# Kernel optimization log

Measured on AMD Instinct MI355X. Metric: run time of the kernel, lower is better.

The kernel has to match this reference:

```python
import jax, jax.numpy as jnp
import numpy as np

W_DIM = 72  # positional_encoding(3 coords, 12 freqs) -> 3*12*2
_F1 = np.array([1.0, 3.0, 3.0, 1.0], dtype=np.float32)
_F2 = np.outer(_F1, _F1); _F2 = _F2 / _F2.sum()  # normalized StyleGAN resample filter


def upsample2x(x):
    """Antialiased 2x upsample: zero-insertion + 4-tap [1,3,3,1] FIR, gain=4 (upfirdn2d)."""
    C = x.shape[1]
    k = jnp.tile(jnp.asarray(_F2 * 4.0, x.dtype)[None, None], (C, 1, 1, 1))  # [C,1,4,4]
    return jax.lax.conv_general_dilated(
        x, k, (1, 1), ((2, 2), (2, 2)), lhs_dilation=(2, 2),
        feature_group_count=C, dimension_numbers=('NCHW', 'OIHW', 'NCHW'))


def affine(w_vec, aw, ab):
    # FullyConnectedLayer: runtime weight gain 1/sqrt(w_dim), bias init 1
    return (w_vec @ aw.T) / np.sqrt(W_DIM) + ab


def mod_conv(x, weight, styles, demodulate=True, padding=1):
    """StyleGAN2 modulated conv2d (batch=1). weight [Co,Ci,k,k], styles [Ci]."""
    w = weight * styles[None, :, None, None]
    if demodulate:
        d = jax.lax.rsqrt(jnp.sum(w * w, axis=(1, 2, 3)) + 1e-8)
        w = w * d[:, None, None, None]
    return jax.lax.conv_general_dilated(
        x, w, (1, 1), ((padding, padding), (padding, padding)),
        dimension_numbers=('NCHW', 'OIHW', 'NCHW'))


def syn_layer(x, w_vec, aw, ab, cw, cb, up):
    s = affine(w_vec, aw, ab)
    if up:
        x = upsample2x(x)
    x = mod_conv(x, cw, s, True, 1)
    # bias_act: lrelu, gain sqrt(2), conv_clamp 256 (noise_strength init 0 -> no noise)
    x = jax.nn.leaky_relu(x + cb[None, :, None, None], 0.2) * np.sqrt(2.0)
    return jnp.clip(x, -256.0, 256.0)


def to_rgb(x, w_vec, aw, ab, cw, cb):
    s = affine(w_vec, aw, ab) / np.sqrt(cw.shape[1])  # ToRGB weight_gain 1/sqrt(Cin)
    y = mod_conv(x, cw, s, False, 0)
    return jnp.clip(y + cb[None, :, None, None], -256.0, 256.0)


def reference(rays, rgbs, conv_w, conv_b, bn_gamma, bn_beta, bn_mean, bn_var,
              a0_w, a0_b, w0, b0, a1_w, a1_b, w1, b1, t0_aw, t0_ab, t0_w, t0_b,
              a2_w, a2_b, w2, b2, a3_w, a3_b, w3, b3, t1_aw, t1_ab, t1_w, t1_b):
    # style vector from positional encoding of ray origin
    p = rays[0, :3, 0, 0]
    fb = 2.0 ** jnp.arange(12, dtype=rays.dtype)
    pts = (p[:, None] * fb[None, :]).reshape(-1)  # (36,)
    w_vec = jnp.concatenate([jnp.sin(pts), jnp.cos(pts)])  # (72,)
    # mapping: 1x1 conv + relu + BatchNorm2d (eval-mode)
    feat = jnp.einsum('oi,bihw->bohw', conv_w[:, :, 0, 0], rgbs) + conv_b[None, :, None, None]
    feat = jax.nn.relu(feat)
    inv = jax.lax.rsqrt(bn_var + 1e-5)
    feat = (feat - bn_mean[None, :, None, None]) * (inv * bn_gamma)[None, :, None, None] + bn_beta[None, :, None, None]
    rgb = feat[:, :3]
    # block0: 32ch@128 -> 256ch@256, skip-architecture ToRGB
    x = syn_layer(feat, w_vec, a0_w, a0_b, w0, b0, True)
    x = syn_layer(x, w_vec, a1_w, a1_b, w1, b1, False)
    img = upsample2x(rgb) + to_rgb(x, w_vec, t0_aw, t0_ab, t0_w, t0_b)
    # block1: 256ch@256 -> 128ch@512
    x = syn_layer(x, w_vec, a2_w, a2_b, w2, b2, True)
    x = syn_layer(x, w_vec, a3_w, a3_b, w3, b3, False)
    img = upsample2x(img) + to_rgb(x, w_vec, t1_aw, t1_ab, t1_w, t1_b)
    return img  # [1,3,512,512]


def setup_inputs() -> dict:
    key = jax.random.key(0)
    ks = jax.random.split(key, 16)
    rn = lambda k, s: jax.random.normal(k, s, dtype=jnp.float32)
    z = lambda s: jnp.zeros(s, jnp.float32)
    o = lambda s: jnp.ones(s, jnp.float32)
    inp = {}
    inp['rays'] = rn(ks[0], (1, 6, 128, 128))
    inp['rgbs'] = jax.random.uniform(ks[1], (1, 3, 128, 128), dtype=jnp.float32)
    inp['conv_w'] = rn(ks[2], (32, 3, 1, 1)); inp['conv_b'] = z((32,))
    inp['bn_gamma'] = o((32,)); inp['bn_beta'] = z((32,))
    inp['bn_mean'] = z((32,)); inp['bn_var'] = o((32,))
    inp['a0_w'] = rn(ks[3], (32, 72)); inp['a0_b'] = o((32,))
    inp['w0'] = rn(ks[4], (256, 32, 3, 3)); inp['b0'] = z((256,))
    inp['a1_w'] = rn(ks[5], (256, 72)); inp['a1_b'] = o((256,))
    inp['w1'] = rn(ks[6], (256, 256, 3, 3)); inp['b1'] = z((256,))
    inp['t0_aw'] = rn(ks[7], (256, 72)); inp['t0_ab'] = o((256,))
    inp['t0_w'] = rn(ks[8], (3, 256, 1, 1)); inp['t0_b'] = z((3,))
    inp['a2_w'] = rn(ks[9], (256, 72)); inp['a2_b'] = o((256,))
    inp['w2'] = rn(ks[10], (128, 256, 3, 3)); inp['b2'] = z((128,))
    inp['a3_w'] = rn(ks[11], (128, 72)); inp['a3_b'] = o((128,))
    inp['w3'] = rn(ks[12], (128, 128, 3, 3)); inp['b3'] = z((128,))
    inp['t1_aw'] = rn(ks[13], (128, 72)); inp['t1_ab'] = o((128,))
    inp['t1_w'] = rn(ks[14], (3, 128, 1, 1)); inp['t1_b'] = z((3,))
    return inp
```

## Files before the change

### kernel.cpp

```cpp
#include <hip/hip_runtime.h>
#include <cstddef>

typedef __attribute__((ext_vector_type(8))) short short8;
typedef __attribute__((ext_vector_type(4))) float f32x4;
typedef __attribute__((address_space(3))) void lds_void;
typedef const __attribute__((address_space(1))) void glob_void;

static const size_t OFF_S0    = 0;
static const size_t OFF_S1    = 64;
static const size_t OFF_S2    = 320;
static const size_t OFF_S3    = 576;
static const size_t OFF_MT0   = 704;
static const size_t OFF_MT1   = 1472;
static const size_t OFF_ZERO  = 1856;
static const size_t OFF_RGBF  = 2048;
static const size_t OFF_IMG0  = 51200;
static const size_t OFF_RGBP  = 247808;
static const size_t OFF_WQ0   = 1900544;
static const size_t OFF_WQ1   = 1937408;
static const size_t OFF_WQ2   = 2232320;
static const size_t OFF_WQ3   = 2379776;
static const size_t OFF_FEAT  = 2453504;
static const size_t OFF_UFEAT = 2715648;
static const size_t OFF_X1    = 4194304;
static const size_t OFF_X2    = 4194304;
static const size_t OFF_U     = 20971520;
static const size_t OFF_X0    = 20971520;

__device__ __forceinline__ unsigned short f2bf(float f) {
  unsigned int u = __float_as_uint(f);
  return (unsigned short)((u + 0x7FFFu + ((u >> 16) & 1u)) >> 16);
}
__device__ __forceinline__ float b2f(short h) {
  return __uint_as_float(((unsigned int)(unsigned short)h) << 16);
}

__global__ void __launch_bounds__(256) prep_kernel(
    const float* __restrict__ rays,
    const float* __restrict__ a0w, const float* __restrict__ a0b,
    const float* __restrict__ a1w, const float* __restrict__ a1b,
    const float* __restrict__ t0aw, const float* __restrict__ t0ab,
    const float* __restrict__ a2w, const float* __restrict__ a2b,
    const float* __restrict__ a3w, const float* __restrict__ a3b,
    const float* __restrict__ t1aw, const float* __restrict__ t1ab,
    const float* __restrict__ t0w, const float* __restrict__ t1w,
    float* __restrict__ ws)
{
  __shared__ float wv[72];
  __shared__ float st0l[256];
  __shared__ float st1l[128];
  const int tid = threadIdx.x;
  if (tid < 128) ws[OFF_ZERO + tid] = 0.f;
  if (tid < 36) {
    int i = tid / 12, j = tid % 12;
    float v = rays[i * 16384] * (float)(1 << j);
    wv[tid]      = sinf(v);
    wv[36 + tid] = cosf(v);
  }
  __syncthreads();
  const float inv72 = 0.11785113019775793f;

  if (tid < 32) {
    float d = 0.f;
    for (int k = 0; k < 72; ++k) d += wv[k] * a0w[tid * 72 + k];
    ws[OFF_S0 + tid] = fmaf(d, inv72, a0b[tid]);
  }
  {
    float d = 0.f;
    for (int k = 0; k < 72; ++k) d += wv[k] * a1w[tid * 72 + k];
    ws[OFF_S1 + tid] = fmaf(d, inv72, a1b[tid]);
  }
  {
    float d = 0.f;
    for (int k = 0; k < 72; ++k) d += wv[k] * t0aw[tid * 72 + k];
    st0l[tid] = fmaf(d, inv72, t0ab[tid]) * 0.0625f;
  }
  {
    float d = 0.f;
    for (int k = 0; k < 72; ++k) d += wv[k] * a2w[tid * 72 + k];
    ws[OFF_S2 + tid] = fmaf(d, inv72, a2b[tid]);
  }
  if (tid < 128) {
    float d = 0.f;
    for (int k = 0; k < 72; ++k) d += wv[k] * a3w[tid * 72 + k];
    ws[OFF_S3 + tid] = fmaf(d, inv72, a3b[tid]);
  }
  if (tid < 128) {
    float d = 0.f;
    for (int k = 0; k < 72; ++k) d += wv[k] * t1aw[tid * 72 + k];
    st1l[tid] = fmaf(d, inv72, t1ab[tid]) * 0.08838834764831845f;
  }
  __syncthreads();
  for (int i = tid; i < 768; i += 256) ws[OFF_MT0 + i] = t0w[i] * st0l[i & 255];
  for (int i = tid; i < 384; i += 256) ws[OFF_MT1 + i] = t1w[i] * st1l[i & 127];
}

__global__ void __launch_bounds__(256) modw_kernel(
    const float* __restrict__ w, const float* __restrict__ s,
    unsigned short* __restrict__ wq, int Ci, int Co)
{
  const int co = blockIdx.x;
  const int n = Ci * 9;
  float local = 0.f;
  for (int i = threadIdx.x; i < n; i += 256) {
    float v = w[co * n + i] * s[i / 9];
    local += v * v;
  }
#pragma unroll
  for (int off = 32; off >= 1; off >>= 1) local += __shfl_xor(local, off);
  __shared__ float red[4];
  if ((threadIdx.x & 63) == 0) red[threadIdx.x >> 6] = local;
  __syncthreads();
  const float d = rsqrtf(red[0] + red[1] + red[2] + red[3] + 1e-8f);
  const int sxor = (co & 3) ^ ((co >> 2) & 3);
  for (int i = threadIdx.x; i < n; i += 256) {
    int ci = i / 9, t = i - ci * 9;
    int kk = ci & 31;
    int sl = (kk >> 3) ^ sxor;
    wq[(((size_t)(ci >> 5) * 9 + t) * Co + co) * 32 + (sl << 3) + (kk & 7)] =
        f2bf(w[co * n + i] * s[ci] * d);
  }
}

__global__ void __launch_bounds__(256) feat_kernel(
    const float* __restrict__ rgbs, const float* __restrict__ cw, const float* __restrict__ cb,
    const float* __restrict__ gam, const float* __restrict__ bet,
    const float* __restrict__ mean, const float* __restrict__ var,
    unsigned short* __restrict__ feat, float* __restrict__ rgbf)
{
  const int p = blockIdx.x * 256 + threadIdx.x;
  const float r = rgbs[p], g = rgbs[16384 + p], b = rgbs[32768 + p];
  unsigned int pk[16];
#pragma unroll
  for (int co = 0; co < 32; ++co) {
    float v = cw[co * 3] * r + cw[co * 3 + 1] * g + cw[co * 3 + 2] * b + cb[co];
    v = fmaxf(v, 0.f);
    float inv = rsqrtf(var[co] + 1e-5f);
    v = (v - mean[co]) * (inv * gam[co]) + bet[co];
    if (co < 3) rgbf[co * 16384 + p] = v;
    unsigned int h = f2bf(v);
    if ((co & 1) == 0) pk[co >> 1] = h;
    else               pk[co >> 1] |= h << 16;
  }
  uint4* dst = reinterpret_cast<uint4*>(feat + (size_t)p * 32);
#pragma unroll
  for (int q = 0; q < 4; ++q)
    dst[q] = make_uint4(pk[q * 4], pk[q * 4 + 1], pk[q * 4 + 2], pk[q * 4 + 3]);
}

__global__ void __launch_bounds__(256) up2x_nhwc_kernel(
    const unsigned short* __restrict__ in, unsigned short* __restrict__ out,
    int H, int W, int c8s , int w2s )
{
  const int cid = blockIdx.x * 256 + threadIdx.x;
  const int k = cid & ((1 << c8s) - 1);
  const int pix = cid >> c8s;
  const int ey = pix >> w2s;
  const int ex = pix & ((1 << w2s) - 1);
  const int C = 8 << c8s;
  int ry0; float ay0, ay1;
  if (ey & 1) { ry0 = ey >> 1;       ay0 = 0.75f; ay1 = 0.25f; }
  else        { ry0 = (ey >> 1) - 1; ay0 = 0.25f; ay1 = 0.75f; }
  int cx0; float bx0, bx1;
  if (ex & 1) { cx0 = ex >> 1;       bx0 = 0.75f; bx1 = 0.25f; }
  else        { cx0 = (ex >> 1) - 1; bx0 = 0.25f; bx1 = 0.75f; }
  const short8 z = {0, 0, 0, 0, 0, 0, 0, 0};
  short8 v00 = z, v01 = z, v10 = z, v11 = z;
  const bool yo0 = (ry0 >= 0), yo1 = (ry0 + 1 < H);
  const bool xo0 = (cx0 >= 0), xo1 = (cx0 + 1 < W);
  if (yo0 && xo0) v00 = *reinterpret_cast<const short8*>(in + ((size_t)(ry0 * W + cx0) * C + k * 8));
  if (yo0 && xo1) v01 = *reinterpret_cast<const short8*>(in + ((size_t)(ry0 * W + cx0 + 1) * C + k * 8));
  if (yo1 && xo0) v10 = *reinterpret_cast<const short8*>(in + ((size_t)((ry0 + 1) * W + cx0) * C + k * 8));
  if (yo1 && xo1) v11 = *reinterpret_cast<const short8*>(in + ((size_t)((ry0 + 1) * W + cx0 + 1) * C + k * 8));
  unsigned int o[4];
#pragma unroll
  for (int j = 0; j < 8; ++j) {
    float f = ay0 * (bx0 * b2f(v00[j]) + bx1 * b2f(v01[j]))
            + ay1 * (bx0 * b2f(v10[j]) + bx1 * b2f(v11[j]));
    unsigned int h = f2bf(f);
    if ((j & 1) == 0) o[j >> 1] = h;
    else              o[j >> 1] |= h << 16;
  }
  *reinterpret_cast<uint4*>(out + (size_t)pix * C + k * 8) = make_uint4(o[0], o[1], o[2], o[3]);
}

template <bool FUSE_RGB>
__global__ void __launch_bounds__(512) conv3x3_mfma(
    const unsigned short* __restrict__ in,
    const unsigned short* __restrict__ wq,
    const float* __restrict__ bias,
    unsigned short* __restrict__ out,
    const float* __restrict__ rgbw,
    float* __restrict__ rgbp,
    const unsigned short* __restrict__ zpage,
    int H, int W, int Ci, int Co)
{
  const int tid  = threadIdx.x;
  const int lane = tid & 63;
  const int wv   = tid >> 6;
  const int wr   = wv & 3;
  const int wg   = wv >> 2;
  const int lo   = lane & 15, hi = lane >> 4;
  const int tpr  = W >> 4;
  const int T_y  = (blockIdx.x / tpr) << 5;
  const int T_x  = (blockIdx.x % tpr) << 4;
  const int cogB = blockIdx.y << 7;
  const int cog  = cogB + (wg << 6);

  __shared__ short8 xs[2][2448];
  __shared__ short8 wlds[2][1536];
  __shared__ float  rw[FUSE_RGB ? 384 : 4];

  if (FUSE_RGB) {
    for (int i = tid; i < 3 * Co; i += 512) rw[i] = rgbw[i];
  }

  f32x4 acc[4][8];
#pragma unroll
  for (int a = 0; a < 4; ++a)
#pragma unroll
    for (int b = 0; b < 8; ++b) acc[a][b] = (f32x4){0.f, 0.f, 0.f, 0.f};

  const unsigned short* gsrc[5];
#pragma unroll
  for (int j = 0; j < 5; ++j) {
    const int s = j * 512 + tid;
    const int pix = s >> 2, kslot = s & 3;
    const int rr = pix / 18, cc = pix - rr * 18;
    const int gy = T_y - 1 + rr, gx = T_x - 1 + cc;
    const int k = kslot ^ ((cc >> 1) & 3);
    const bool inb = (s < 2448) && gy >= 0 && gy < H && gx >= 0 && gx < W;
    gsrc[j] = inb ? (in + ((size_t)(gy * W + gx) * Ci + (k << 3))) : zpage;
  }

#define STAGE(c, buf)                                                              \
  {                                                                                \
    const int cb_ = (c) << 5;                                                      \
    _Pragma("unroll")                                                              \
    for (int j = 0; j < 4; ++j)                                                    \
      __builtin_amdgcn_global_load_lds((glob_void*)(gsrc[j] + cb_),                \
                                       (lds_void*)&xs[buf][j * 512 + tid], 16, 0, 0); \
    if (tid < 400)                                                                 \
      __builtin_amdgcn_global_load_lds((glob_void*)(gsrc[4] + cb_),                \
                                       (lds_void*)&xs[buf][2048 + tid], 16, 0, 0); \
  }

#define STAGE_W(C, KX, BUF)                                                        \
  {                                                                                \
    _Pragma("unroll")                                                              \
    for (int j = 0; j < 3; ++j) {                                                  \
      const unsigned short* src_ =                                                 \
          wq + ((size_t)((C) * 9 + j * 3 + (KX)) * Co + cogB) * 32 + tid * 8;      \
      __builtin_amdgcn_global_load_lds((glob_void*)src_,                           \
                                       (lds_void*)&wlds[BUF][(j << 9) + tid], 16, 0, 0); \
    }                                                                              \
  }

  const int sxa   = (lo & 3) ^ ((lo >> 2) & 3);
  const int wbase = (((wg << 6) + lo) << 2) + (hi ^ sxa);
#define ALOADW(SLOT, KY, BUF)                                                      \
  {                                                                                \
    _Pragma("unroll")                                                              \
    for (int cf = 0; cf < 4; ++cf)                                                 \
      apf[SLOT][cf] = wlds[BUF][((KY) << 9) + wbase + (cf << 6)];                  \
  }

#define MF(A, B, C) __builtin_amdgcn_mfma_f32_16x16x32_bf16(A, B, C, 0, 0, 0)

  STAGE(0, 0);
  STAGE_W(0, 0, 0);
  __syncthreads();

  const int nch = Ci >> 5;
  const int rstride = 72;
  int wb = 0;
  for (int c = 0; c < nch; ++c) {
    const int cur = c & 1;
#pragma unroll
    for (int g = 0; g < 3; ++g) {
      if (g < 2)             { STAGE_W(c, g + 1, wb ^ 1); }
      else if (c + 1 < nch)  { STAGE_W(c + 1, 0, wb ^ 1); }
      if (g == 0 && c + 1 < nch) STAGE(c + 1, cur ^ 1);

      const int tx2  = lo + g;
      const int xv_  = hi ^ ((tx2 >> 1) & 3);
      const int rowb = (((wr << 3) * 18 + tx2) << 2) + xv_;

      short8 q0 = xs[cur][rowb];
      short8 q1 = xs[cur][rowb + rstride];
      short8 q2 = xs[cur][rowb + 2 * rstride];
      short8 q3 = xs[cur][rowb + 3 * rstride];
      short8 q4 = xs[cur][rowb + 4 * rstride];
      short8 q5 = xs[cur][rowb + 5 * rstride];
      short8 q6 = xs[cur][rowb + 6 * rstride];
      short8 q7 = xs[cur][rowb + 7 * rstride];

      short8 apf[2][4];
      ALOADW(0, 0, wb);
      ALOADW(1, 1, wb);
#pragma unroll
      for (int cf = 0; cf < 4; ++cf) {
        acc[cf][0] = MF(apf[0][cf], q0, acc[cf][0]);
        acc[cf][1] = MF(apf[0][cf], q1, acc[cf][1]);
        acc[cf][2] = MF(apf[0][cf], q2, acc[cf][2]);
        acc[cf][3] = MF(apf[0][cf], q3, acc[cf][3]);
        acc[cf][4] = MF(apf[0][cf], q4, acc[cf][4]);
        acc[cf][5] = MF(apf[0][cf], q5, acc[cf][5]);
        acc[cf][6] = MF(apf[0][cf], q6, acc[cf][6]);
        acc[cf][7] = MF(apf[0][cf], q7, acc[cf][7]);
      }
      short8 q8 = xs[cur][rowb + 8 * rstride];
      ALOADW(0, 2, wb);
#pragma unroll
      for (int cf = 0; cf < 4; ++cf) {
        acc[cf][0] = MF(apf[1][cf], q1, acc[cf][0]);
        acc[cf][1] = MF(apf[1][cf], q2, acc[cf][1]);
        acc[cf][2] = MF(apf[1][cf], q3, acc[cf][2]);
        acc[cf][3] = MF(apf[1][cf], q4, acc[cf][3]);
        acc[cf][4] = MF(apf[1][cf], q5, acc[cf][4]);
        acc[cf][5] = MF(apf[1][cf], q6, acc[cf][5]);
        acc[cf][6] = MF(apf[1][cf], q7, acc[cf][6]);
        acc[cf][7] = MF(apf[1][cf], q8, acc[cf][7]);
      }
      short8 q9 = xs[cur][rowb + 9 * rstride];
#pragma unroll
      for (int cf = 0; cf < 4; ++cf) {
        acc[cf][0] = MF(apf[0][cf], q2, acc[cf][0]);
        acc[cf][1] = MF(apf[0][cf], q3, acc[cf][1]);
        acc[cf][2] = MF(apf[0][cf], q4, acc[cf][2]);
        acc[cf][3] = MF(apf[0][cf], q5, acc[cf][3]);
        acc[cf][4] = MF(apf[0][cf], q6, acc[cf][4]);
        acc[cf][5] = MF(apf[0][cf], q7, acc[cf][5]);
        acc[cf][6] = MF(apf[0][cf], q8, acc[cf][6]);
        acc[cf][7] = MF(apf[0][cf], q9, acc[cf][7]);
      }
      __syncthreads();
      wb ^= 1;
    }
  }
#undef STAGE
#undef STAGE_W
#undef ALOADW
#undef MF

  const float rt2 = 1.41421356237309515f;
#pragma unroll
  for (int r = 0; r < 8; ++r) {
    const int gy = T_y + (wr << 3) + r;
    const int gx = T_x + lo;
    if (!FUSE_RGB) {
#pragma unroll
      for (int cf = 0; cf < 4; ++cf) {
        const int cb = cog + (cf << 4) + (hi << 2);
        const f32x4 bi = *reinterpret_cast<const f32x4*>(bias + cb);
        unsigned short h[4];
#pragma unroll
        for (int reg = 0; reg < 4; ++reg) {
          float vv = acc[cf][r][reg] + bi[reg];
          vv = (vv >= 0.f) ? vv : 0.2f * vv;
          vv *= rt2;
          vv = fminf(fmaxf(vv, -256.f), 256.f);
          h[reg] = f2bf(vv);
        }
        uint2 pk;
        pk.x = (unsigned int)h[0] | ((unsigned int)h[1] << 16);
        pk.y = (unsigned int)h[2] | ((unsigned int)h[3] << 16);
        *reinterpret_cast<uint2*>(out + (size_t)(gy * W + gx) * Co + cb) = pk;
      }
    } else {
      float p0 = 0.f, p1 = 0.f, p2 = 0.f;
#pragma unroll
      for (int cf = 0; cf < 4; ++cf) {
        const int cb = cog + (cf << 4) + (hi << 2);
        const f32x4 bi = *reinterpret_cast<const f32x4*>(bias + cb);
#pragma unroll
        for (int reg = 0; reg < 4; ++reg) {
          float vv = acc[cf][r][reg] + bi[reg];
          vv = (vv >= 0.f) ? vv : 0.2f * vv;
          vv *= rt2;
          vv = fminf(fmaxf(vv, -256.f), 256.f);
          p0 = fmaf(rw[cb + reg], vv, p0);
          p1 = fmaf(rw[Co + cb + reg], vv, p1);
          p2 = fmaf(rw[2 * Co + cb + reg], vv, p2);
        }
      }
      p0 += __shfl_xor(p0, 16); p0 += __shfl_xor(p0, 32);
      p1 += __shfl_xor(p1, 16); p1 += __shfl_xor(p1, 32);
      p2 += __shfl_xor(p2, 16); p2 += __shfl_xor(p2, 32);
      if (hi == 0) {
        const size_t HWs = (size_t)H * W;
        const size_t px  = (size_t)gy * W + gx;
        rgbp[((size_t)wg * 3 + 0) * HWs + px] = p0;
        rgbp[((size_t)wg * 3 + 1) * HWs + px] = p1;
        rgbp[((size_t)wg * 3 + 2) * HWs + px] = p2;
      }
    }
  }
}

__device__ __forceinline__ float up2x_sample(const float* __restrict__ im, int H, int W,
                                             int oy, int ox)
{
  int my = oy >> 1, mx = ox >> 1;
  int ry0; float ay0, ay1;
  if (oy & 1) { ry0 = my;     ay0 = 0.75f; ay1 = 0.25f; }
  else        { ry0 = my - 1; ay0 = 0.25f; ay1 = 0.75f; }
  int cx0; float bx0, bx1;
  if (ox & 1) { cx0 = mx;     bx0 = 0.75f; bx1 = 0.25f; }
  else        { cx0 = mx - 1; bx0 = 0.25f; bx1 = 0.75f; }
  float v00 = (ry0 >= 0    && cx0 >= 0   ) ? im[ry0 * W + cx0]           : 0.f;
  float v01 = (ry0 >= 0    && cx0 + 1 < W) ? im[ry0 * W + cx0 + 1]       : 0.f;
  float v10 = (ry0 + 1 < H && cx0 >= 0   ) ? im[(ry0 + 1) * W + cx0]     : 0.f;
  float v11 = (ry0 + 1 < H && cx0 + 1 < W) ? im[(ry0 + 1) * W + cx0 + 1] : 0.f;
  return ay0 * (bx0 * v00 + bx1 * v01) + ay1 * (bx0 * v10 + bx1 * v11);
}

__global__ void __launch_bounds__(256) img0_kernel(
    const float* __restrict__ rgbf, const unsigned short* __restrict__ x1,
    const float* __restrict__ mt0g, const float* __restrict__ tb,
    float* __restrict__ img0)
{
  __shared__ float mt[768];
  const int tid = threadIdx.x;
  for (int i = tid; i < 768; i += 256) mt[i] = mt0g[i];
  __syncthreads();
  const int p = blockIdx.x * 256 + tid;
  const unsigned short* xp = x1 + (size_t)p * 256;
  float a0 = 0.f, a1 = 0.f, a2 = 0.f;
  for (int i8 = 0; i8 < 32; ++i8) {
    const short8 v = *reinterpret_cast<const short8*>(xp + i8 * 8);
#pragma unroll
    for (int j = 0; j < 8; ++j) {
      const float xv = b2f(v[j]);
      const int ci = i8 * 8 + j;
      a0 = fmaf(mt[ci],       xv, a0);
      a1 = fmaf(mt[256 + ci], xv, a1);
      a2 = fmaf(mt[512 + ci], xv, a2);
    }
  }
  const int oy = p >> 8, ox = p & 255;
  float av[3] = {a0, a1, a2};
#pragma unroll
  for (int o = 0; o < 3; ++o) {
    float y = fminf(fmaxf(av[o] + tb[o], -256.f), 256.f);
    img0[o * 65536 + p] = up2x_sample(rgbf + o * 16384, 128, 128, oy, ox) + y;
  }
}

__global__ void __launch_bounds__(256) final_kernel(
    const float* __restrict__ img0, const float* __restrict__ rgbp,
    const float* __restrict__ tb, float* __restrict__ out)
{
  const int p = blockIdx.x * 256 + threadIdx.x;
  const int oy = p >> 9, ox = p & 511;
#pragma unroll
  for (int o = 0; o < 3; ++o) {
    float a = rgbp[(0 * 3 + o) * 262144 + p] + rgbp[(1 * 3 + o) * 262144 + p];
    float y = fminf(fmaxf(a + tb[o], -256.f), 256.f);
    out[o * 262144 + p] = up2x_sample(img0 + o * 65536, 256, 256, oy, ox) + y;
  }
}

extern "C" void kernel_launch(void* const* d_in, const int* in_sizes, int n_in,
                              void* d_out, int out_size, void* d_ws, size_t ws_size,
                              hipStream_t stream)
{
  const float* rays   = (const float*)d_in[0];
  const float* rgbs   = (const float*)d_in[1];
  const float* conv_w = (const float*)d_in[2];
  const float* conv_b = (const float*)d_in[3];
  const float* bn_g   = (const float*)d_in[4];
  const float* bn_b   = (const float*)d_in[5];
  const float* bn_m   = (const float*)d_in[6];
  const float* bn_v   = (const float*)d_in[7];
  const float* a0_w   = (const float*)d_in[8];
  const float* a0_b   = (const float*)d_in[9];
  const float* w0     = (const float*)d_in[10];
  const float* b0     = (const float*)d_in[11];
  const float* a1_w   = (const float*)d_in[12];
  const float* a1_b   = (const float*)d_in[13];
  const float* w1     = (const float*)d_in[14];
  const float* b1     = (const float*)d_in[15];
  const float* t0_aw  = (const float*)d_in[16];
  const float* t0_ab  = (const float*)d_in[17];
  const float* t0_w   = (const float*)d_in[18];
  const float* t0_b   = (const float*)d_in[19];
  const float* a2_w   = (const float*)d_in[20];
  const float* a2_b   = (const float*)d_in[21];
  const float* w2     = (const float*)d_in[22];
  const float* b2     = (const float*)d_in[23];
  const float* a3_w   = (const float*)d_in[24];
  const float* a3_b   = (const float*)d_in[25];
  const float* w3     = (const float*)d_in[26];
  const float* b3     = (const float*)d_in[27];
  const float* t1_aw  = (const float*)d_in[28];
  const float* t1_ab  = (const float*)d_in[29];
  const float* t1_w   = (const float*)d_in[30];
  const float* t1_b   = (const float*)d_in[31];

  float* ws  = (float*)d_ws;
  float* out = (float*)d_out;

  unsigned short* wq0   = (unsigned short*)(ws + OFF_WQ0);
  unsigned short* wq1   = (unsigned short*)(ws + OFF_WQ1);
  unsigned short* wq2   = (unsigned short*)(ws + OFF_WQ2);
  unsigned short* wq3   = (unsigned short*)(ws + OFF_WQ3);
  unsigned short* featb = (unsigned short*)(ws + OFF_FEAT);
  unsigned short* ufeat = (unsigned short*)(ws + OFF_UFEAT);
  unsigned short* x0b   = (unsigned short*)(ws + OFF_X0);
  unsigned short* x1b   = (unsigned short*)(ws + OFF_X1);
  unsigned short* x2b   = (unsigned short*)(ws + OFF_X2);
  unsigned short* Ub    = (unsigned short*)(ws + OFF_U);
  const unsigned short* zpage = (const unsigned short*)(ws + OFF_ZERO);

  prep_kernel<<<1, 256, 0, stream>>>(rays, a0_w, a0_b, a1_w, a1_b, t0_aw, t0_ab,
                                     a2_w, a2_b, a3_w, a3_b, t1_aw, t1_ab,
                                     t0_w, t1_w, ws);
  modw_kernel<<<256, 256, 0, stream>>>(w0, ws + OFF_S0, wq0, 32, 256);
  modw_kernel<<<256, 256, 0, stream>>>(w1, ws + OFF_S1, wq1, 256, 256);
  modw_kernel<<<128, 256, 0, stream>>>(w2, ws + OFF_S2, wq2, 256, 128);
  modw_kernel<<<128, 256, 0, stream>>>(w3, ws + OFF_S3, wq3, 128, 128);
  feat_kernel<<<64, 256, 0, stream>>>(rgbs, conv_w, conv_b, bn_g, bn_b, bn_m, bn_v,
                                      featb, ws + OFF_RGBF);
  up2x_nhwc_kernel<<<1024, 256, 0, stream>>>(featb, ufeat, 128, 128, 2, 8);
  conv3x3_mfma<false><<<dim3(128, 2), 512, 0, stream>>>(
      ufeat, wq0, b0, x0b, nullptr, nullptr, zpage, 256, 256, 32, 256);
  conv3x3_mfma<false><<<dim3(128, 2), 512, 0, stream>>>(
      x0b, wq1, b1, x1b, nullptr, nullptr, zpage, 256, 256, 256, 256);
  img0_kernel<<<256, 256, 0, stream>>>(ws + OFF_RGBF, x1b, ws + OFF_MT0, t0_b,
                                       ws + OFF_IMG0);
  up2x_nhwc_kernel<<<32768, 256, 0, stream>>>(x1b, Ub, 256, 256, 5, 9);
  conv3x3_mfma<false><<<dim3(512, 1), 512, 0, stream>>>(
      Ub, wq2, b2, x2b, nullptr, nullptr, zpage, 512, 512, 256, 128);
  conv3x3_mfma<true><<<dim3(512, 1), 512, 0, stream>>>(
      x2b, wq3, b3, nullptr, ws + OFF_MT1, ws + OFF_RGBP, zpage, 512, 512, 128, 128);
  final_kernel<<<1024, 256, 0, stream>>>(ws + OFF_IMG0, ws + OFF_RGBP, t1_b, out);
}
```

Baseline: 409.5 us.

## Triple-buffer conv weights with counted vmcnt waits and MFMA priority hints

The 3x3 conv main loop now uses three weight LDS buffers, one per kx slice, and issues all weight and next-chunk input loads up front. The full __syncthreads after each group is replaced with partial s_waitcnt vmcnt counts plus raw barriers, so later loads can stay in flight while earlier groups compute. MFMA blocks are wrapped in s_setprio raises, and the input staging is made unconditional by padding the LDS tile to 2560 entries. The costs are more LDS use, which may reduce occupancy, and hand-counted vmcnt values that depend on the exact load issue order, so any miscount could cause races. On the last chunk the loop also issues redundant loads that wrap around to chunk 0.

```diff
diff --git a/kernel.cpp b/kernel.cpp
--- a/kernel.cpp
+++ b/kernel.cpp
@@ -207,8 +207,8 @@
   const int cogB = blockIdx.y << 7;
   const int cog  = cogB + (wg << 6);
 
-  __shared__ short8 xs[2][2448];
-  __shared__ short8 wlds[2][1536];
+  __shared__ short8 xs[2][2560];
+  __shared__ short8 wlds[3][1536];
   __shared__ float  rw[FUSE_RGB ? 384 : 4];
 
   if (FUSE_RGB) {
@@ -237,12 +237,9 @@
   {                                                                                \
     const int cb_ = (c) << 5;                                                      \
     _Pragma("unroll")                                                              \
-    for (int j = 0; j < 4; ++j)                                                    \
+    for (int j = 0; j < 5; ++j)                                                    \
       __builtin_amdgcn_global_load_lds((glob_void*)(gsrc[j] + cb_),                \
                                        (lds_void*)&xs[buf][j * 512 + tid], 16, 0, 0); \
-    if (tid < 400)                                                                 \
-      __builtin_amdgcn_global_load_lds((glob_void*)(gsrc[4] + cb_),                \
-                                       (lds_void*)&xs[buf][2048 + tid], 16, 0, 0); \
   }
 
 #define STAGE_W(C, KX, BUF)                                                        \
@@ -267,81 +264,97 @@
 
 #define MF(A, B, C) __builtin_amdgcn_mfma_f32_16x16x32_bf16(A, B, C, 0, 0, 0)
 
+#define COMPUTE_GROUP(G)                                                           \
+  {                                                                                \
+    const int tx2  = lo + (G);                                                     \
+    const int xv_  = hi ^ ((tx2 >> 1) & 3);                                        \
+    const int rowb = (((wr << 3) * 18 + tx2) << 2) + xv_;                          \
+    short8 q0 = xs[cur][rowb];                                                     \
+    short8 q1 = xs[cur][rowb + 72];                                                \
+    short8 q2 = xs[cur][rowb + 2 * 72];                                            \
+    short8 q3 = xs[cur][rowb + 3 * 72];                                            \
+    short8 q4 = xs[cur][rowb + 4 * 72];                                            \
+    short8 q5 = xs[cur][rowb + 5 * 72];                                            \
+    short8 q6 = xs[cur][rowb + 6 * 72];                                            \
+    short8 q7 = xs[cur][rowb + 7 * 72];                                            \
+    short8 apf[2][4];                                                              \
+    ALOADW(0, 0, G);                                                               \
+    ALOADW(1, 1, G);                                                               \
+    __builtin_amdgcn_s_setprio(1);                                                 \
+    _Pragma("unroll")                                                              \
+    for (int cf = 0; cf < 4; ++cf) {                                               \
+      acc[cf][0] = MF(apf[0][cf], q0, acc[cf][0]);                                 \
+      acc[cf][1] = MF(apf[0][cf], q1, acc[cf][1]);                                 \
+      acc[cf][2] = MF(apf[0][cf], q2, acc[cf][2]);                                 \
+      acc[cf][3] = MF(apf[0][cf], q3, acc[cf][3]);                                 \
+      acc[cf][4] = MF(apf[0][cf], q4, acc[cf][4]);                                 \
+      acc[cf][5] = MF(apf[0][cf], q5, acc[cf][5]);                                 \
+      acc[cf][6] = MF(apf[0][cf], q6, acc[cf][6]);                                 \
+      acc[cf][7] = MF(apf[0][cf], q7, acc[cf][7]);                                 \
+    }                                                                              \
+    __builtin_amdgcn_s_setprio(0);                                                 \
+    short8 q8 = xs[cur][rowb + 8 * 72];                                            \
+    ALOADW(0, 2, G);                                                               \
+    __builtin_amdgcn_s_setprio(1);                                                 \
+    _Pragma("unroll")                                                              \
+    for (int cf = 0; cf < 4; ++cf) {                                               \
+      acc[cf][0] = MF(apf[1][cf], q1, acc[cf][0]);                                 \
+      acc[cf][1] = MF(apf[1][cf], q2, acc[cf][1]);                                 \
+      acc[cf][2] = MF(apf[1][cf], q3, acc[cf][2]);                                 \
+      acc[cf][3] = MF(apf[1][cf], q4, acc[cf][3]);                                 \
+      acc[cf][4] = MF(apf[1][cf], q5, acc[cf][4]);                                 \
+      acc[cf][5] = MF(apf[1][cf], q6, acc[cf][5]);                                 \
+      acc[cf][6] = MF(apf[1][cf], q7, acc[cf][6]);                                 \
+      acc[cf][7] = MF(apf[1][cf], q8, acc[cf][7]);                                 \
+    }                                                                              \
+    __builtin_amdgcn_s_setprio(0);                                                 \
+    short8 q9 = xs[cur][rowb + 9 * 72];                                            \
+    __builtin_amdgcn_s_setprio(1);                                                 \
+    _Pragma("unroll")                                                              \
+    for (int cf = 0; cf < 4; ++cf) {                                               \
+      acc[cf][0] = MF(apf[0][cf], q2, acc[cf][0]);                                 \
+      acc[cf][1] = MF(apf[0][cf], q3, acc[cf][1]);                                 \
+      acc[cf][2] = MF(apf[0][cf], q4, acc[cf][2]);                                 \
+      acc[cf][3] = MF(apf[0][cf], q5, acc[cf][3]);                                 \
+      acc[cf][4] = MF(apf[0][cf], q6, acc[cf][4]);                                 \
+      acc[cf][5] = MF(apf[0][cf], q7, acc[cf][5]);                                 \
+      acc[cf][6] = MF(apf[0][cf], q8, acc[cf][6]);                                 \
+      acc[cf][7] = MF(apf[0][cf], q9, acc[cf][7]);                                 \
+    }                                                                              \
+    __builtin_amdgcn_s_setprio(0);                                                 \
+  }
+
   STAGE(0, 0);
   STAGE_W(0, 0, 0);
-  __syncthreads();
+  asm volatile("s_waitcnt vmcnt(0) lgkmcnt(0)" ::: "memory");
+  __builtin_amdgcn_s_barrier();
 
   const int nch = Ci >> 5;
-  const int rstride = 72;
-  int wb = 0;
   for (int c = 0; c < nch; ++c) {
     const int cur = c & 1;
-#pragma unroll
-    for (int g = 0; g < 3; ++g) {
-      if (g < 2)             { STAGE_W(c, g + 1, wb ^ 1); }
-      else if (c + 1 < nch)  { STAGE_W(c + 1, 0, wb ^ 1); }
-      if (g == 0 && c + 1 < nch) STAGE(c + 1, cur ^ 1);
-
-      const int tx2  = lo + g;
-      const int xv_  = hi ^ ((tx2 >> 1) & 3);
-      const int rowb = (((wr << 3) * 18 + tx2) << 2) + xv_;
-
-      short8 q0 = xs[cur][rowb];
-      short8 q1 = xs[cur][rowb + rstride];
-      short8 q2 = xs[cur][rowb + 2 * rstride];
-      short8 q3 = xs[cur][rowb + 3 * rstride];
-      short8 q4 = xs[cur][rowb + 4 * rstride];
-      short8 q5 = xs[cur][rowb + 5 * rstride];
-      short8 q6 = xs[cur][rowb + 6 * rstride];
-      short8 q7 = xs[cur][rowb + 7 * rstride];
-
-      short8 apf[2][4];
-      ALOADW(0, 0, wb);
-      ALOADW(1, 1, wb);
-#pragma unroll
-      for (int cf = 0; cf < 4; ++cf) {
-        acc[cf][0] = MF(apf[0][cf], q0, acc[cf][0]);
-        acc[cf][1] = MF(apf[0][cf], q1, acc[cf][1]);
-        acc[cf][2] = MF(apf[0][cf], q2, acc[cf][2]);
-        acc[cf][3] = MF(apf[0][cf], q3, acc[cf][3]);
-        acc[cf][4] = MF(apf[0][cf], q4, acc[cf][4]);
-        acc[cf][5] = MF(apf[0][cf], q5, acc[cf][5]);
-        acc[cf][6] = MF(apf[0][cf], q6, acc[cf][6]);
-        acc[cf][7] = MF(apf[0][cf], q7, acc[cf][7]);
-      }
-      short8 q8 = xs[cur][rowb + 8 * rstride];
-      ALOADW(0, 2, wb);
-#pragma unroll
-      for (int cf = 0; cf < 4; ++cf) {
-        acc[cf][0] = MF(apf[1][cf], q1, acc[cf][0]);
-        acc[cf][1] = MF(apf[1][cf], q2, acc[cf][1]);
-        acc[cf][2] = MF(apf[1][cf], q3, acc[cf][2]);
-        acc[cf][3] = MF(apf[1][cf], q4, acc[cf][3]);
-        acc[cf][4] = MF(apf[1][cf], q5, acc[cf][4]);
-        acc[cf][5] = MF(apf[1][cf], q6, acc[cf][5]);
-        acc[cf][6] = MF(apf[1][cf], q7, acc[cf][6]);
-        acc[cf][7] = MF(apf[1][cf], q8, acc[cf][7]);
-      }
-      short8 q9 = xs[cur][rowb + 9 * rstride];
-#pragma unroll
-      for (int cf = 0; cf < 4; ++cf) {
-        acc[cf][0] = MF(apf[0][cf], q2, acc[cf][0]);
-        acc[cf][1] = MF(apf[0][cf], q3, acc[cf][1]);
-        acc[cf][2] = MF(apf[0][cf], q4, acc[cf][2]);
-        acc[cf][3] = MF(apf[0][cf], q5, acc[cf][3]);
-        acc[cf][4] = MF(apf[0][cf], q6, acc[cf][4]);
-        acc[cf][5] = MF(apf[0][cf], q7, acc[cf][5]);
-        acc[cf][6] = MF(apf[0][cf], q8, acc[cf][6]);
-        acc[cf][7] = MF(apf[0][cf], q9, acc[cf][7]);
-      }
-      __syncthreads();
-      wb ^= 1;
-    }
+    const int cnext = (c + 1 < nch) ? (c + 1) : 0;
+
+    STAGE_W(c, 1, 1);
+    STAGE_W(c, 2, 2);
+    STAGE(cnext, cur ^ 1);
+    COMPUTE_GROUP(0)
+    asm volatile("s_waitcnt vmcnt(8)" ::: "memory");
+    __builtin_amdgcn_s_barrier();
+
+    COMPUTE_GROUP(1)
+    asm volatile("s_waitcnt vmcnt(5)" ::: "memory");
+    __builtin_amdgcn_s_barrier();
+
+    STAGE_W(cnext, 0, 0);
+    COMPUTE_GROUP(2)
+    asm volatile("s_waitcnt vmcnt(0)" ::: "memory");
+    __builtin_amdgcn_s_barrier();
   }
 #undef STAGE
 #undef STAGE_W
 #undef ALOADW
 #undef MF
+#undef COMPUTE_GROUP
 
   const float rt2 = 1.41421356237309515f;
 #pragma unroll
```

Measured after the change: 406.7 us, median of 3. Within noise of the previous version (-0.7%).
